# Kernel optimization log

Measured on AMD Instinct MI355X. Metric: run time of the kernel, lower is better.

The kernel has to match this reference:

```python
import jax, jax.numpy as jnp
import numpy as np

D_MODEL = 1024
N_HEADS = 16
HEAD_DIM = D_MODEL // N_HEADS
SCALE = float(np.sqrt(HEAD_DIM))


def setup_inputs() -> dict:
    key = jax.random.key(0)
    ks = jax.random.split(key, 12)
    B, S, D = 4, 2048, D_MODEL
    std = 1.0 / np.sqrt(D)
    inp = {
        "query": jax.random.normal(ks[0], (B, S, D), jnp.float32),
        "key": jax.random.normal(ks[1], (B, S, D), jnp.float32),
        "value": jax.random.normal(ks[2], (B, S, D), jnp.float32),
        "wq_w": jax.random.normal(ks[3], (D, D), jnp.float32) * std,
        "wq_b": jnp.zeros((D,), jnp.float32),
        "wk_w": jax.random.normal(ks[4], (D, D), jnp.float32) * std,
        "wk_b": jnp.zeros((D,), jnp.float32),
        "wv_w": jax.random.normal(ks[5], (D, D), jnp.float32) * std,
        "wv_b": jnp.zeros((D,), jnp.float32),
        "fc_w": jax.random.normal(ks[6], (D, D), jnp.float32) * std,
        "fc_b": jnp.zeros((D,), jnp.float32),
    }
    return inp


def reference(query, key, value, wq_w, wq_b, wk_w, wk_b, wv_w, wv_b, fc_w, fc_b):
    B, S, D = query.shape
    H, Hd = N_HEADS, HEAD_DIM
    # QKV projections (torch Linear: x @ W.T + b)
    Q = query @ wq_w.T + wq_b
    K = key @ wk_w.T + wk_b
    V = value @ wv_w.T + wv_b
    # [B, H, S, Hd]
    Q = Q.reshape(B, S, H, Hd).transpose(0, 2, 1, 3)
    K = K.reshape(B, S, H, Hd).transpose(0, 2, 1, 3)
    V = V.reshape(B, S, H, Hd).transpose(0, 2, 1, 3)
    energy = jnp.einsum("bhqd,bhkd->bhqk", Q, K) / SCALE
    attention = jax.nn.softmax(energy, axis=-1)  # dropout=0 (eval)
    weighted = jnp.einsum("bhqk,bhkd->bhqd", attention, V)
    weighted = weighted.transpose(0, 2, 1, 3).reshape(B, S, D)
    output = weighted @ fc_w.T + fc_b
    return (output, attention)
```

## Files before the change

### kernel.cpp

```cpp
#include <hip/hip_runtime.h>
#include <hip/hip_bf16.h>

typedef __attribute__((ext_vector_type(8))) short short8;
typedef __attribute__((ext_vector_type(4))) short short4v;
typedef __attribute__((ext_vector_type(4))) float float4v;

#define GLD_LDS(g, l) __builtin_amdgcn_global_load_lds( \
    (const __attribute__((address_space(1))) void*)(g), \
    (__attribute__((address_space(3))) void*)(l), 16, 0, 0)

__device__ __forceinline__ short f2bf(float x) {
  __hip_bfloat16 h = __float2bfloat16(x);
  return __builtin_bit_cast(short, h);
}

__global__ __launch_bounds__(256) void cast3(
    const float4v* __restrict__ in0, const float4v* __restrict__ in1,
    const float4v* __restrict__ in2,
    short4v* __restrict__ o0, short4v* __restrict__ o1, short4v* __restrict__ o2,
    int n4)
{
  const float4v* in = blockIdx.y == 0 ? in0 : blockIdx.y == 1 ? in1 : in2;
  short4v* out = blockIdx.y == 0 ? o0 : blockIdx.y == 1 ? o1 : o2;
  int i = blockIdx.x * 256 + threadIdx.x;
  if (i < n4) {
    float4v v = in[i];
    short4v o;
    o[0] = f2bf(v[0]); o[1] = f2bf(v[1]); o[2] = f2bf(v[2]); o[3] = f2bf(v[3]);
    out[i] = o;
  }
}

__global__ __launch_bounds__(256) void cast4(
    const float4v* __restrict__ in0, const float4v* __restrict__ in1,
    const float4v* __restrict__ in2, const float4v* __restrict__ in3,
    short4v* __restrict__ o0, short4v* __restrict__ o1,
    short4v* __restrict__ o2, short4v* __restrict__ o3,
    int n4)
{
  const float4v* in = blockIdx.y == 0 ? in0 : blockIdx.y == 1 ? in1
                    : blockIdx.y == 2 ? in2 : in3;
  short4v* out = blockIdx.y == 0 ? o0 : blockIdx.y == 1 ? o1
               : blockIdx.y == 2 ? o2 : o3;
  int i = blockIdx.x * 256 + threadIdx.x;
  if (i < n4) {
    float4v v = in[i];
    short4v o;
    o[0] = f2bf(v[0]); o[1] = f2bf(v[1]); o[2] = f2bf(v[2]); o[3] = f2bf(v[3]);
    out[i] = o;
  }
}

template<int MODE>
__global__ __launch_bounds__(256) void gemm_bt(
    const short* __restrict__ A, const short* __restrict__ B,
    const float* __restrict__ bias, void* __restrict__ Cv,
    int M, int N, int K)
{
  __shared__ short As[2][128 * 64];
  __shared__ short Bs[2][128 * 64];
  const int tid = threadIdx.x;
  const int w = tid >> 6, lane = tid & 63;
  const int g = lane >> 4, cc = lane & 15;
  const int m0 = blockIdx.x * 128, n0 = blockIdx.y * 128;
  const int wr = (w >> 1) * 64, wc = (w & 1) * 64;

  float4v acc[4][4];
#pragma unroll
  for (int mi = 0; mi < 4; ++mi)
#pragma unroll
    for (int ni = 0; ni < 4; ++ni)
      acc[mi][ni] = (float4v){0.f, 0.f, 0.f, 0.f};

  const int cbase0 = w * 64;
  const int row_l[4] = {(cbase0 + lane) >> 3, (256 + cbase0 + lane) >> 3,
                        (512 + cbase0 + lane) >> 3, (768 + cbase0 + lane) >> 3};
  const int col_l = ((lane) & 7) * 8;

  auto stage = [&](int buf, int k0) {
#pragma unroll
    for (int i = 0; i < 4; ++i) {
      int cbase = i * 256 + cbase0;
      GLD_LDS(A + (long)(m0 + row_l[i]) * K + k0 + col_l, &As[buf][cbase * 8]);
      GLD_LDS(B + (long)(n0 + row_l[i]) * K + k0 + col_l, &Bs[buf][cbase * 8]);
    }
  };
  auto compute = [&](int buf) {
#pragma unroll
    for (int ks = 0; ks < 2; ++ks) {
      short8 af[4], bfr[4];
#pragma unroll
      for (int mi = 0; mi < 4; ++mi)
        af[mi] = *(const short8*)&As[buf][(wr + mi * 16 + cc) * 64 + ks * 32 + g * 8];
#pragma unroll
      for (int ni = 0; ni < 4; ++ni)
        bfr[ni] = *(const short8*)&Bs[buf][(wc + ni * 16 + cc) * 64 + ks * 32 + g * 8];
#pragma unroll
      for (int mi = 0; mi < 4; ++mi)
#pragma unroll
        for (int ni = 0; ni < 4; ++ni)
          acc[mi][ni] = __builtin_amdgcn_mfma_f32_16x16x32_bf16(
              af[mi], bfr[ni], acc[mi][ni], 0, 0, 0);
    }
  };

  stage(0, 0);
  __syncthreads();
#pragma unroll 1
  for (int k0 = 0; k0 < K; k0 += 128) {
    stage(1, k0 + 64);
    compute(0);
    __syncthreads();
    if (k0 + 128 < K) stage(0, k0 + 128);
    compute(1);
    __syncthreads();
  }

#pragma unroll
  for (int mi = 0; mi < 4; ++mi) {
#pragma unroll
    for (int ni = 0; ni < 4; ++ni) {
      int mb = m0 + wr + mi * 16 + g * 4;
      int nn = n0 + wc + ni * 16 + cc;
      float4v v = acc[mi][ni];
      if constexpr (MODE == 0) {
        float bb = bias[nn];
        __hip_bfloat16* C = (__hip_bfloat16*)Cv;
#pragma unroll
        for (int r = 0; r < 4; ++r)
          C[(long)(mb + r) * N + nn] = __float2bfloat16(v[r] + bb);
      } else if constexpr (MODE == 1) {
        __hip_bfloat16* C = (__hip_bfloat16*)Cv;
        long base = (long)(nn >> 11) * 2097152 + (nn & 2047);
#pragma unroll
        for (int r = 0; r < 4; ++r)
          C[(long)(mb + r) * 2048 + base] = __float2bfloat16(v[r] + bias[mb + r]);
      } else {
        float bb = bias[nn];
        float* C = (float*)Cv;
#pragma unroll
        for (int r = 0; r < 4; ++r)
          C[(long)(mb + r) * N + nn] = v[r] + bb;
      }
    }
  }
}

__global__ __launch_bounds__(256) void attn_fwd(
    const short* __restrict__ Qb, const short* __restrict__ Kb,
    const short* __restrict__ VTb, float* __restrict__ attn_out,
    __hip_bfloat16* __restrict__ Wout)
{
  __shared__ short plds[4][32][72];
  const int S = 2048, D = 1024;
  const int bh = blockIdx.y, b = bh >> 4, h = bh & 15;
  const int tid = threadIdx.x, w = tid >> 6, lane = tid & 63;
  const int g = lane >> 4, cc = lane & 15;
  const int q0 = blockIdx.x * 128 + w * 32;

  const short* Qp = Qb + (long)b * S * D + h * 64;
  const short* Kp = Kb + (long)b * S * D + h * 64;
  const short* Vt = VTb + (long)bh * 64 * S;

  short8 qf[2][2];
#pragma unroll
  for (int mi = 0; mi < 2; ++mi)
#pragma unroll
    for (int ks = 0; ks < 2; ++ks)
      qf[mi][ks] = *(const short8*)(Qp + (long)(q0 + mi * 16 + cc) * D + ks * 32 + g * 8);

  float l[2] = {0.f, 0.f};
  const float SC = 0.125f;

#pragma unroll 1
  for (int kt = 0; kt < S; kt += 64) {
    float4v e[2][4];
#pragma unroll
    for (int mi = 0; mi < 2; ++mi)
#pragma unroll
      for (int ni = 0; ni < 4; ++ni) e[mi][ni] = (float4v){0.f, 0.f, 0.f, 0.f};
#pragma unroll
    for (int ks = 0; ks < 2; ++ks) {
      short8 kf[4];
#pragma unroll
      for (int ni = 0; ni < 4; ++ni)
        kf[ni] = *(const short8*)(Kp + (long)(kt + ni * 16 + cc) * D + ks * 32 + g * 8);
#pragma unroll
      for (int mi = 0; mi < 2; ++mi)
#pragma unroll
        for (int ni = 0; ni < 4; ++ni)
          e[mi][ni] = __builtin_amdgcn_mfma_f32_16x16x32_bf16(
              kf[ni], qf[mi][ks], e[mi][ni], 0, 0, 0);
    }
#pragma unroll
    for (int mi = 0; mi < 2; ++mi)
#pragma unroll
      for (int ni = 0; ni < 4; ++ni)
#pragma unroll
        for (int r = 0; r < 4; ++r)
          l[mi] += __expf(e[mi][ni][r] * SC);
  }
  float rl[2];
#pragma unroll
  for (int mi = 0; mi < 2; ++mi) {
    float s = l[mi];
    s += __shfl_xor(s, 16);
    s += __shfl_xor(s, 32);
    rl[mi] = 1.0f / s;
  }

  float4v Wacc[2][4];
#pragma unroll
  for (int mi = 0; mi < 2; ++mi)
#pragma unroll
    for (int ni = 0; ni < 4; ++ni) Wacc[mi][ni] = (float4v){0.f, 0.f, 0.f, 0.f};

  float* Arow = attn_out + (long)bh * S * S;
#pragma unroll 1
  for (int kt = 0; kt < S; kt += 64) {
    float4v e[2][4];
#pragma unroll
    for (int mi = 0; mi < 2; ++mi)
#pragma unroll
      for (int ni = 0; ni < 4; ++ni) e[mi][ni] = (float4v){0.f, 0.f, 0.f, 0.f};
#pragma unroll
    for (int ks = 0; ks < 2; ++ks) {
      short8 kf[4];
#pragma unroll
      for (int ni = 0; ni < 4; ++ni)
        kf[ni] = *(const short8*)(Kp + (long)(kt + ni * 16 + cc) * D + ks * 32 + g * 8);
#pragma unroll
      for (int mi = 0; mi < 2; ++mi)
#pragma unroll
        for (int ni = 0; ni < 4; ++ni)
          e[mi][ni] = __builtin_amdgcn_mfma_f32_16x16x32_bf16(
              kf[ni], qf[mi][ks], e[mi][ni], 0, 0, 0);
    }
#pragma unroll
    for (int mi = 0; mi < 2; ++mi) {
#pragma unroll
      for (int ni = 0; ni < 4; ++ni) {
        float4v pv;
#pragma unroll
        for (int r = 0; r < 4; ++r)
          pv[r] = __expf(e[mi][ni][r] * SC) * rl[mi];
        __builtin_nontemporal_store(
            pv, (float4v*)(Arow + (long)(q0 + mi * 16 + cc) * S + kt + ni * 16 + g * 4));
        short4v pb;
#pragma unroll
        for (int r = 0; r < 4; ++r) pb[r] = f2bf(pv[r]);
        *(short4v*)&plds[w][mi * 16 + cc][ni * 16 + g * 4] = pb;
      }
    }
#pragma unroll
    for (int ks = 0; ks < 2; ++ks) {
      short8 pa[2], vf[4];
#pragma unroll
      for (int mi = 0; mi < 2; ++mi)
        pa[mi] = *(const short8*)&plds[w][mi * 16 + cc][ks * 32 + g * 8];
#pragma unroll
      for (int ni = 0; ni < 4; ++ni)
        vf[ni] = *(const short8*)(Vt + (long)(ni * 16 + cc) * S + kt + ks * 32 + g * 8);
#pragma unroll
      for (int mi = 0; mi < 2; ++mi)
#pragma unroll
        for (int ni = 0; ni < 4; ++ni)
          Wacc[mi][ni] = __builtin_amdgcn_mfma_f32_16x16x32_bf16(
              pa[mi], vf[ni], Wacc[mi][ni], 0, 0, 0);
    }
  }

#pragma unroll
  for (int mi = 0; mi < 2; ++mi)
#pragma unroll
    for (int ni = 0; ni < 4; ++ni)
#pragma unroll
      for (int r = 0; r < 4; ++r)
        Wout[(long)(b * S + q0 + mi * 16 + g * 4 + r) * D + h * 64 + ni * 16 + cc] =
            __float2bfloat16(Wacc[mi][ni][r]);
}

extern "C" void kernel_launch(void* const* d_in, const int* in_sizes, int n_in,
                              void* d_out, int out_size, void* d_ws, size_t ws_size,
                              hipStream_t stream) {
  const float* query = (const float*)d_in[0];
  const float* key   = (const float*)d_in[1];
  const float* value = (const float*)d_in[2];
  const float* wq_w  = (const float*)d_in[3];
  const float* wq_b  = (const float*)d_in[4];
  const float* wk_w  = (const float*)d_in[5];
  const float* wk_b  = (const float*)d_in[6];
  const float* wv_w  = (const float*)d_in[7];
  const float* wv_b  = (const float*)d_in[8];
  const float* fc_w  = (const float*)d_in[9];
  const float* fc_b  = (const float*)d_in[10];

  char* ws = (char*)d_ws;
  short* Qb  = (short*)(ws);
  short* Kb  = (short*)(ws + 16777216);
  short* VT  = (short*)(ws + 33554432);
  short* Wq  = (short*)(ws + 50331648);
  short* Wk  = (short*)(ws + 52428800);
  short* Wv  = (short*)(ws + 54525952);
  short* Wfc = (short*)(ws + 56623104);
  short* Xq  = (short*)(ws + 58720256);
  short* Xk  = (short*)(ws + 75497472);
  short* Xv  = (short*)(ws + 92274688);
  short* Wgt = Xq;

  float* out0 = (float*)d_out;
  float* attn_out = out0 + 8388608;

  cast3<<<dim3(8192, 3), 256, 0, stream>>>(
      (const float4v*)query, (const float4v*)key, (const float4v*)value,
      (short4v*)Xq, (short4v*)Xk, (short4v*)Xv, 2097152);
  cast4<<<dim3(1024, 4), 256, 0, stream>>>(
      (const float4v*)wq_w, (const float4v*)wk_w, (const float4v*)wv_w,
      (const float4v*)fc_w,
      (short4v*)Wq, (short4v*)Wk, (short4v*)Wv, (short4v*)Wfc, 262144);

  gemm_bt<0><<<dim3(64, 8), 256, 0, stream>>>(Xq, Wq, wq_b, Qb, 8192, 1024, 1024);
  gemm_bt<0><<<dim3(64, 8), 256, 0, stream>>>(Xk, Wk, wk_b, Kb, 8192, 1024, 1024);
  gemm_bt<1><<<dim3(8, 64), 256, 0, stream>>>(Wv, Xv, wv_b, VT, 1024, 8192, 1024);

  attn_fwd<<<dim3(16, 64), 256, 0, stream>>>(Qb, Kb, VT, attn_out,
                                             (__hip_bfloat16*)Wgt);

  gemm_bt<2><<<dim3(64, 8), 256, 0, stream>>>(Wgt, Wfc, fc_b, out0, 8192, 1024, 1024);
}
```

Measured before the change: 597.0 us.

## Swizzle GEMM and attention block order, use exp2 with folded normalization, set priorities

Block indices in the GEMM are remapped into grouped supertiles so neighbouring blocks share A/B tiles in cache. In attention, the head index now varies fastest so blocks that share K/V run together. Softmax uses exp2 with a pre-scaled constant and folds the reciprocal sum into the exponent as a log2 offset, which removes a multiply per element. The stores of the attention matrix are no longer nontemporal, and s_setprio is raised around the MFMA sections. Together these target cache locality, ALU work and wave scheduling, at some risk of small numeric differences and more cache pollution from the regular stores.

```diff
diff --git a/kernel.cpp b/kernel.cpp
--- a/kernel.cpp
+++ b/kernel.cpp
@@ -1,5 +1,6 @@
 #include <hip/hip_runtime.h>
 #include <hip/hip_bf16.h>
+#include <math.h>
 
 typedef __attribute__((ext_vector_type(8))) short short8;
 typedef __attribute__((ext_vector_type(4))) short short4v;
@@ -62,7 +63,18 @@
   const int tid = threadIdx.x;
   const int w = tid >> 6, lane = tid & 63;
   const int g = lane >> 4, cc = lane & 15;
-  const int m0 = blockIdx.x * 128, n0 = blockIdx.y * 128;
+
+  const int GM = gridDim.x, GN = gridDim.y;
+  const int bid = blockIdx.x + GM * blockIdx.y;
+  const int sm = (GM >= GN) ? 4 : 8;
+  const int sn = 32 / sm;
+  const int st = bid >> 5, is = bid & 31;
+  const int mi_s = is % sm, ni_s = is / sm;
+  const int stiles_n = GN / sn;
+  const int st_m = st / stiles_n, st_n = st % stiles_n;
+  const int m0 = (st_m * sm + mi_s) * 128;
+  const int n0 = (st_n * sn + ni_s) * 128;
+
   const int wr = (w >> 1) * 64, wc = (w & 1) * 64;
 
   float4v acc[4][4];
@@ -75,7 +87,7 @@
   const int cbase0 = w * 64;
   const int row_l[4] = {(cbase0 + lane) >> 3, (256 + cbase0 + lane) >> 3,
                         (512 + cbase0 + lane) >> 3, (768 + cbase0 + lane) >> 3};
-  const int col_l = ((lane) & 7) * 8;
+  const int col_l = (lane & 7) * 8;
 
   auto stage = [&](int buf, int k0) {
 #pragma unroll
@@ -153,10 +165,12 @@
 {
   __shared__ short plds[4][32][72];
   const int S = 2048, D = 1024;
-  const int bh = blockIdx.y, b = bh >> 4, h = bh & 15;
+  const int bid = blockIdx.x + (blockIdx.y << 4);
+  const int bh = bid & 63, b = bh >> 4, h = bh & 15;
+  const int qi = bid >> 6;
   const int tid = threadIdx.x, w = tid >> 6, lane = tid & 63;
   const int g = lane >> 4, cc = lane & 15;
-  const int q0 = blockIdx.x * 128 + w * 32;
+  const int q0 = qi * 128 + w * 32;
 
   const short* Qp = Qb + (long)b * S * D + h * 64;
   const short* Kp = Kb + (long)b * S * D + h * 64;
@@ -170,7 +184,7 @@
       qf[mi][ks] = *(const short8*)(Qp + (long)(q0 + mi * 16 + cc) * D + ks * 32 + g * 8);
 
   float l[2] = {0.f, 0.f};
-  const float SC = 0.125f;
+  const float C2 = 0.18033688011112042f;
 
 #pragma unroll 1
   for (int kt = 0; kt < S; kt += 64) {
@@ -179,6 +193,7 @@
     for (int mi = 0; mi < 2; ++mi)
 #pragma unroll
       for (int ni = 0; ni < 4; ++ni) e[mi][ni] = (float4v){0.f, 0.f, 0.f, 0.f};
+    __builtin_amdgcn_s_setprio(1);
 #pragma unroll
     for (int ks = 0; ks < 2; ++ks) {
       short8 kf[4];
@@ -192,21 +207,23 @@
           e[mi][ni] = __builtin_amdgcn_mfma_f32_16x16x32_bf16(
               kf[ni], qf[mi][ks], e[mi][ni], 0, 0, 0);
     }
+    __builtin_amdgcn_s_setprio(0);
 #pragma unroll
     for (int mi = 0; mi < 2; ++mi)
 #pragma unroll
       for (int ni = 0; ni < 4; ++ni)
 #pragma unroll
         for (int r = 0; r < 4; ++r)
-          l[mi] += __expf(e[mi][ni][r] * SC);
-  }
-  float rl[2];
+          l[mi] += __builtin_exp2f(e[mi][ni][r] * C2);
+  }
+  float rl[2], lrl[2];
 #pragma unroll
   for (int mi = 0; mi < 2; ++mi) {
     float s = l[mi];
     s += __shfl_xor(s, 16);
     s += __shfl_xor(s, 32);
     rl[mi] = 1.0f / s;
+    lrl[mi] = -__log2f(s);
   }
 
   float4v Wacc[2][4];
@@ -223,6 +240,7 @@
     for (int mi = 0; mi < 2; ++mi)
 #pragma unroll
       for (int ni = 0; ni < 4; ++ni) e[mi][ni] = (float4v){0.f, 0.f, 0.f, 0.f};
+    __builtin_amdgcn_s_setprio(1);
 #pragma unroll
     for (int ks = 0; ks < 2; ++ks) {
       short8 kf[4];
@@ -236,6 +254,7 @@
           e[mi][ni] = __builtin_amdgcn_mfma_f32_16x16x32_bf16(
               kf[ni], qf[mi][ks], e[mi][ni], 0, 0, 0);
     }
+    __builtin_amdgcn_s_setprio(0);
 #pragma unroll
     for (int mi = 0; mi < 2; ++mi) {
 #pragma unroll
@@ -243,15 +262,15 @@
         float4v pv;
 #pragma unroll
         for (int r = 0; r < 4; ++r)
-          pv[r] = __expf(e[mi][ni][r] * SC) * rl[mi];
-        __builtin_nontemporal_store(
-            pv, (float4v*)(Arow + (long)(q0 + mi * 16 + cc) * S + kt + ni * 16 + g * 4));
+          pv[r] = __builtin_exp2f(__builtin_fmaf(e[mi][ni][r], C2, lrl[mi]));
+        *(float4v*)(Arow + (long)(q0 + mi * 16 + cc) * S + kt + ni * 16 + g * 4) = pv;
         short4v pb;
 #pragma unroll
         for (int r = 0; r < 4; ++r) pb[r] = f2bf(pv[r]);
         *(short4v*)&plds[w][mi * 16 + cc][ni * 16 + g * 4] = pb;
       }
     }
+    __builtin_amdgcn_s_setprio(1);
 #pragma unroll
     for (int ks = 0; ks < 2; ++ks) {
       short8 pa[2], vf[4];
@@ -268,6 +287,7 @@
           Wacc[mi][ni] = __builtin_amdgcn_mfma_f32_16x16x32_bf16(
               pa[mi], vf[ni], Wacc[mi][ni], 0, 0, 0);
     }
+    __builtin_amdgcn_s_setprio(0);
   }
 
 #pragma unroll
@@ -278,6 +298,7 @@
       for (int r = 0; r < 4; ++r)
         Wout[(long)(b * S + q0 + mi * 16 + g * 4 + r) * D + h * 64 + ni * 16 + cc] =
             __float2bfloat16(Wacc[mi][ni][r]);
+  (void)rl;
 }
 
 extern "C" void kernel_launch(void* const* d_in, const int* in_sizes, int n_in,
```

New measurement: 723.3 us. 21.2% more time.
